# Kernel optimization log

Hardware: AMD Instinct MI355X
Metric: run time of the kernel (lower is better)

The kernel has to match this reference:

```python
import jax, jax.numpy as jnp
import numpy as np

N_USERS = 50000
N_ENT = 100000
N_NODES = N_USERS + N_ENT
N_EDGES = 2400000
EMB = 64
LAYER_DIMS = [(64, 64), (64, 32), (32, 16)]  # (in_dim, out_dim) per layer


def setup_inputs() -> dict:
    key = jax.random.key(0)
    ks = jax.random.split(key, 20)
    inp = {
        'user_embed': jax.random.normal(ks[0], (N_USERS, EMB), jnp.float32) * 0.1,
        'entity_embed': jax.random.normal(ks[1], (N_ENT, EMB), jnp.float32) * 0.1,
        'edge_val': jax.random.uniform(ks[2], (N_EDGES,), jnp.float32),
        'edge_row': jax.random.randint(ks[3], (N_EDGES,), 0, N_NODES),
        'edge_col': jax.random.randint(ks[4], (N_EDGES,), 0, N_NODES),
    }
    i = 5
    for k, (din, dout) in enumerate(LAYER_DIMS):
        scale = float(np.sqrt(6.0 / (din + dout)))  # xavier_uniform
        inp[f'W_gc_{k}'] = jax.random.uniform(ks[i], (din, dout), jnp.float32, -scale, scale); i += 1
        inp[f'b_gc_{k}'] = jnp.zeros((dout,), jnp.float32)
        inp[f'W_bi_{k}'] = jax.random.uniform(ks[i], (din, dout), jnp.float32, -scale, scale); i += 1
        inp[f'b_bi_{k}'] = jnp.zeros((dout,), jnp.float32)
    return inp


def _l2_normalize(x):
    # matches F.normalize(x, p=2, dim=1) with eps=1e-12
    return x / jnp.maximum(jnp.linalg.norm(x, axis=1, keepdims=True), 1e-12)


def reference(user_embed, entity_embed, edge_val, edge_row, edge_col,
              W_gc_0, b_gc_0, W_bi_0, b_bi_0,
              W_gc_1, b_gc_1, W_bi_1, b_bi_1,
              W_gc_2, b_gc_2, W_bi_2, b_bi_2):
    layers = [(W_gc_0, b_gc_0, W_bi_0, b_bi_0),
              (W_gc_1, b_gc_1, W_bi_1, b_bi_1),
              (W_gc_2, b_gc_2, W_bi_2, b_bi_2)]
    x = jnp.concatenate([user_embed, entity_embed], axis=0)  # [N, 64]
    all_emb = [x]
    for W_gc, b_gc, W_bi, b_bi in layers:
        # sparse A @ x : gather source features, scale by edge value, segment-sum into rows
        msgs = edge_val[:, None] * x[edge_col]                       # [E, d]
        side = jax.ops.segment_sum(msgs, edge_row, num_segments=N_NODES)  # [N, d]
        sum_emb = jax.nn.leaky_relu((x + side) @ W_gc + b_gc)        # GCN path
        bi_emb = jax.nn.leaky_relu((x * side) @ W_bi + b_bi)         # bi-interaction path
        x = _l2_normalize(sum_emb + bi_emb)                          # dropout p=0 (eval)
        all_emb.append(x)
    all_emb = jnp.concatenate(all_emb, axis=1)  # [N, 64+64+32+16]
    return all_emb[:N_USERS], all_emb[N_USERS:]
```

## Files before the change

### kernel.cpp

```cpp
#include <hip/hip_runtime.h>
#include <hip/hip_fp16.h>

constexpr int N_USERS = 50000;
constexpr int N_ENT   = 100000;
constexpr int N_NODES = 150000;
constexpr int N_EDGES = 2400000;
constexpr int OUT_D   = 176;

constexpr int NBKT      = 293;
constexpr int P1_BLOCKS = 293;
constexpr int CHUNK     = 8192;
constexpr int TBL       = NBKT * P1_BLOCKS;
constexpr int SCAN_BLKS = (TBL + 1023) / 1024;


typedef _Float16 h2v __attribute__((ext_vector_type(2)));
union H2U { unsigned u; h2v v; };

__device__ inline float dot2(unsigned a, unsigned b, float c) {
    H2U x, y; x.u = a; y.u = b;
    return __builtin_amdgcn_fdot2(x.v, y.v, c, false);
}

__global__ __launch_bounds__(256) void init_x_kernel(const float* __restrict__ ue,
                                                     const float* __restrict__ ee,
                                                     float* __restrict__ out,
                                                     __half* __restrict__ xh) {
    int tid = blockIdx.x * 256 + threadIdx.x;
    int n = tid >> 4, q = tid & 15;
    const float* src = (n < N_USERS) ? ue + (size_t)n * 64
                                     : ee + (size_t)(n - N_USERS) * 64;
    float4 v = *(const float4*)(src + q * 4);
    *(float4*)(out + (size_t)n * OUT_D + q * 4) = v;
    union { __half2 h[2]; uint2 u; } pk;
    pk.h[0] = __floats2half2_rn(v.x, v.y);
    pk.h[1] = __floats2half2_rn(v.z, v.w);
    *(uint2*)(xh + (size_t)n * 64 + q * 4) = pk.u;
}

__global__ __launch_bounds__(256) void conv_kernel(const float* __restrict__ src,
                                                   __half* __restrict__ xh, int DIN) {
    int tid = blockIdx.x * 256 + threadIdx.x;
    int n = tid / (DIN / 2), t = tid % (DIN / 2);
    float2 v = *(const float2*)(src + (size_t)n * OUT_D + 2 * t);
    *(__half2*)(xh + (size_t)n * DIN + 2 * t) = __floats2half2_rn(v.x, v.y);
}

__global__ __launch_bounds__(256) void wt_kernel(const float* __restrict__ Wg0,
                                                 const float* __restrict__ Wb0,
                                                 const float* __restrict__ Wg1,
                                                 const float* __restrict__ Wb1,
                                                 const float* __restrict__ Wg2,
                                                 const float* __restrict__ Wb2,
                                                 __half* __restrict__ WT) {
    int idx = blockIdx.x * 256 + threadIdx.x;
    const float* src; int dout, base;
    if (idx < 8192)       { base = (idx < 4096) ? 0 : 4096;
                            src  = (idx < 4096) ? Wg0 : Wb0;  dout = 64; }
    else if (idx < 12288) { base = (idx < 10240) ? 8192 : 10240;
                            src  = (idx < 10240) ? Wg1 : Wb1; dout = 32; }
    else                  { base = (idx < 12800) ? 12288 : 12800;
                            src  = (idx < 12800) ? Wg2 : Wb2; dout = 16; }
    int r = idx - base;
    int i = r / dout, o = r % dout;
    int dest = base + (i / 8) * dout * 8 + o * 8 + (i % 8);
    WT[dest] = __float2half(src[r]);
}

__global__ __launch_bounds__(256) void histP1_kernel(const int* __restrict__ er,
                                                     int* __restrict__ table) {
    __shared__ int h[NBKT];
    for (int i = threadIdx.x; i < NBKT; i += 256) h[i] = 0;
    __syncthreads();
    int base = blockIdx.x * CHUNK;
    for (int i = threadIdx.x; i < CHUNK; i += 256) {
        int e = base + i;
        if (e < N_EDGES) atomicAdd(&h[er[e] >> 9], 1);
    }
    __syncthreads();
    for (int i = threadIdx.x; i < NBKT; i += 256)
        table[i * P1_BLOCKS + blockIdx.x] = h[i];
}

__global__ __launch_bounds__(1024) void scanA_kernel(const int* __restrict__ a,
                                                     int* __restrict__ bsum, int n) {
    __shared__ int wsum[16];
    int i = blockIdx.x * 1024 + threadIdx.x;
    int v = (i < n) ? a[i] : 0;
    #pragma unroll
    for (int off = 32; off; off >>= 1) v += __shfl_xor(v, off);
    int lane = threadIdx.x & 63, w = threadIdx.x >> 6;
    if (lane == 0) wsum[w] = v;
    __syncthreads();
    if (threadIdx.x == 0) {
        int t = 0;
        #pragma unroll
        for (int k = 0; k < 16; ++k) t += wsum[k];
        bsum[blockIdx.x] = t;
    }
}

__global__ __launch_bounds__(1024) void scanB_kernel(int* __restrict__ bsum, int n) {
    __shared__ int wtot[16];
    __shared__ int carry_s;
    int tid = threadIdx.x;
    int lane = tid & 63, w = tid >> 6;
    if (tid == 0) carry_s = 0;
    __syncthreads();
    for (int base = 0; base < n; base += 1024) {
        int i = base + tid;
        int v = (i < n) ? bsum[i] : 0;
        int incl = v;
        #pragma unroll
        for (int off = 1; off < 64; off <<= 1) {
            int t = __shfl_up(incl, off);
            if (lane >= off) incl += t;
        }
        if (lane == 63) wtot[w] = incl;
        __syncthreads();
        int woff = 0, total = 0;
        #pragma unroll
        for (int k = 0; k < 16; ++k) {
            int tk = wtot[k];
            if (k < w) woff += tk;
            total += tk;
        }
        if (i < n) bsum[i] = carry_s + woff + incl - v;
        __syncthreads();
        if (tid == 0) carry_s += total;
        __syncthreads();
    }
}

__global__ __launch_bounds__(1024) void scanC_kernel(int* __restrict__ a,
                                                     const int* __restrict__ bsum, int n) {
    __shared__ int wtot[16];
    int i = blockIdx.x * 1024 + threadIdx.x;
    int lane = threadIdx.x & 63, w = threadIdx.x >> 6;
    int v = (i < n) ? a[i] : 0;
    int incl = v;
    #pragma unroll
    for (int off = 1; off < 64; off <<= 1) {
        int t = __shfl_up(incl, off);
        if (lane >= off) incl += t;
    }
    if (lane == 63) wtot[w] = incl;
    __syncthreads();
    int woff = 0;
    #pragma unroll
    for (int k = 0; k < 16; ++k) if (k < w) woff += wtot[k];
    if (i < n) a[i] = bsum[blockIdx.x] + woff + incl - v;
}

__global__ __launch_bounds__(256) void scatterP1_kernel(const float* __restrict__ ev,
                                                        const int*   __restrict__ er,
                                                        const int*   __restrict__ ec,
                                                        const int*   __restrict__ table,
                                                        unsigned long long* __restrict__ tmp) {
    __shared__ int lcur[NBKT];
    for (int i = threadIdx.x; i < NBKT; i += 256)
        lcur[i] = table[i * P1_BLOCKS + blockIdx.x];
    __syncthreads();
    int base = blockIdx.x * CHUNK;
    for (int i = threadIdx.x; i < CHUNK; i += 256) {
        int e = base + i;
        if (e < N_EDGES) {
            int r = er[e], c = ec[e];
            unsigned hb = (unsigned)__half_as_ushort(__float2half_rn(ev[e]));
            unsigned v14 = (hb + 2u) >> 2;
            int pos = atomicAdd(&lcur[r >> 9], 1);
            tmp[pos] = ((unsigned long long)(r & 511) << 32)
                     | ((unsigned)c << 14) | v14;
        }
    }
}

__global__ __launch_bounds__(512) void pass2_kernel(const unsigned long long* __restrict__ tmp,
                                                    const int* __restrict__ table,
                                                    unsigned* __restrict__ edges,
                                                    int* __restrict__ cursor) {
    __shared__ int hcnt[512];
    __shared__ int sinc[512];
    __shared__ int lcur[512];
    int b = blockIdx.x;
    int tid = threadIdx.x;
    int eStart = table[b * P1_BLOCKS];
    int eEnd = (b + 1 < NBKT) ? table[(b + 1) * P1_BLOCKS] : N_EDGES;

    hcnt[tid] = 0;
    __syncthreads();
    for (int e = eStart + tid; e < eEnd; e += 512)
        atomicAdd(&hcnt[(int)(tmp[e] >> 32)], 1);
    __syncthreads();
    sinc[tid] = hcnt[tid];
    __syncthreads();
    #pragma unroll
    for (int off = 1; off < 512; off <<= 1) {
        int t = (tid >= off) ? sinc[tid - off] : 0;
        __syncthreads();
        sinc[tid] += t;
        __syncthreads();
    }
    int row = b * 512 + tid;
    if (row < N_NODES) cursor[row] = eStart + sinc[tid];
    lcur[tid] = eStart + sinc[tid] - hcnt[tid];
    __syncthreads();
    for (int e = eStart + tid; e < eEnd; e += 512) {
        unsigned long long rec = tmp[e];
        int pos = atomicAdd(&lcur[(int)(rec >> 32)], 1);
        edges[pos] = (unsigned)rec;
    }
}

template<int DIN, int DOUT>
__global__ __launch_bounds__(256, 4) void fused_layer_kernel(
        const int*          __restrict__ cursor,
        const unsigned int* __restrict__ edges,
        const __half*       __restrict__ xh,
        float* __restrict__ out,
        const __half* __restrict__ WT, int wgOff, int wbOff,
        const float* __restrict__ bgc, const float* __restrict__ bbi,
        int cin, int cout) {
    __shared__ unsigned ash[4][DIN / 2];
    __shared__ unsigned bsh[4][DIN / 2];

    int tid = threadIdx.x;
    int w = tid >> 6, lane = tid & 63;
    int n = blockIdx.x * 4 + w;

    constexpr int QP = DIN / 4;
    constexpr int NE = 64 / QP;
    int g = lane / QP;
    int t = lane % QP;

    int s = n ? cursor[n - 1] : 0;
    int e_end = cursor[n];

    float4 xv = make_float4(0.f, 0.f, 0.f, 0.f);
    if (lane < QP) xv = *(const float4*)(out + (size_t)n * OUT_D + cin + 4 * lane);

    const uint2* xq = (const uint2*)xh;
    float fx0 = 0.f, fx1 = 0.f, fx2 = 0.f, fx3 = 0.f;

    for (int e = s; e < e_end; e += 8 * NE) {
        unsigned ue[8];
        #pragma unroll
        for (int j = 0; j < 8; ++j) {
            int i = e + j * NE + g;
            unsigned raw = edges[i];
            ue[j] = (i < e_end) ? raw : 0u;
        }
        uint2 xx[8];
        #pragma unroll
        for (int j = 0; j < 8; ++j)
            xx[j] = xq[(size_t)(ue[j] >> 14) * QP + t];

        __half2 a0 = __floats2half2_rn(0.f, 0.f);
        __half2 a1 = a0;
        #pragma unroll
        for (int j = 0; j < 8; ++j) {
            unsigned bits = (ue[j] & 0x3FFFu) << 2;
            __half vh = __ushort_as_half((unsigned short)bits);
            __half2 vv2 = __half2half2(vh);
            a0 = __hfma2(vv2, *(__half2*)&xx[j].x, a0);
            a1 = __hfma2(vv2, *(__half2*)&xx[j].y, a1);
            if (j == 3 || j == 7) {
                float2 f0 = __half22float2(a0);
                float2 f1 = __half22float2(a1);
                fx0 += f0.x; fx1 += f0.y; fx2 += f1.x; fx3 += f1.y;
                a0 = __floats2half2_rn(0.f, 0.f); a1 = a0;
            }
        }
    }
    #pragma unroll
    for (int m = 32; m >= QP; m >>= 1) {
        fx0 += __shfl_xor(fx0, m);
        fx1 += __shfl_xor(fx1, m);
        fx2 += __shfl_xor(fx2, m);
        fx3 += __shfl_xor(fx3, m);
    }

    if (lane < QP) {
        __half2 a01 = __floats2half2_rn(xv.x + fx0, xv.y + fx1);
        __half2 a23 = __floats2half2_rn(xv.z + fx2, xv.w + fx3);
        __half2 b01 = __floats2half2_rn(xv.x * fx0, xv.y * fx1);
        __half2 b23 = __floats2half2_rn(xv.z * fx2, xv.w * fx3);
        ash[w][2 * lane]     = *(unsigned*)&a01;
        ash[w][2 * lane + 1] = *(unsigned*)&a23;
        bsh[w][2 * lane]     = *(unsigned*)&b01;
        bsh[w][2 * lane + 1] = *(unsigned*)&b23;
    }
    __syncthreads();

    float hres = 0.f;
    if constexpr (DOUT == DIN) {
        int o = lane;
        uint4 wg[DIN / 8], wb[DIN / 8];
        #pragma unroll
        for (int k = 0; k < DIN / 8; ++k) {
            wg[k] = *(const uint4*)(WT + wgOff + (size_t)(k * DOUT + o) * 8);
            wb[k] = *(const uint4*)(WT + wbOff + (size_t)(k * DOUT + o) * 8);
        }
        float ag = bgc[o], ab = bbi[o];
        #pragma unroll
        for (int k = 0; k < DIN / 8; ++k) {
            uint4 a4 = *(const uint4*)&ash[w][k * 4];
            uint4 b4 = *(const uint4*)&bsh[w][k * 4];
            ag = dot2(a4.x, wg[k].x, ag); ag = dot2(a4.y, wg[k].y, ag);
            ag = dot2(a4.z, wg[k].z, ag); ag = dot2(a4.w, wg[k].w, ag);
            ab = dot2(b4.x, wb[k].x, ab); ab = dot2(b4.y, wb[k].y, ab);
            ab = dot2(b4.z, wb[k].z, ab); ab = dot2(b4.w, wb[k].w, ab);
        }
        ag = ag > 0.f ? ag : 0.01f * ag;
        ab = ab > 0.f ? ab : 0.01f * ab;
        hres = ag + ab;
    } else {
        int o = lane & (DOUT - 1);
        bool gc = lane < DOUT;
        bool active = lane < 2 * DOUT;
        int woff2 = gc ? wgOff : wbOff;
        uint4 wr[DIN / 8];
        #pragma unroll
        for (int k = 0; k < DIN / 8; ++k)
            wr[k] = *(const uint4*)(WT + woff2 + (size_t)(k * DOUT + o) * 8);
        const unsigned* sp = gc ? &ash[w][0] : &bsh[w][0];
        float own = active ? (gc ? bgc[o] : bbi[o]) : 0.f;
        #pragma unroll
        for (int k = 0; k < DIN / 8; ++k) {
            uint4 s4 = *(const uint4*)(sp + k * 4);
            own = dot2(s4.x, wr[k].x, own); own = dot2(s4.y, wr[k].y, own);
            own = dot2(s4.z, wr[k].z, own); own = dot2(s4.w, wr[k].w, own);
        }
        own = own > 0.f ? own : 0.01f * own;
        float other = __shfl_xor(own, DOUT);
        hres = own + other;
    }

    float hq = (lane < DOUT) ? hres : 0.f;
    float ss = hq * hq;
    #pragma unroll
    for (int off = 32; off; off >>= 1) ss += __shfl_xor(ss, off);

    if (lane < DOUT) {
        float inv = 1.f / fmaxf(sqrtf(ss), 1e-12f);
        out[(size_t)n * OUT_D + cout + lane] = hres * inv;
    }
}

extern "C" void kernel_launch(void* const* d_in, const int* in_sizes, int n_in,
                              void* d_out, int out_size, void* d_ws, size_t ws_size,
                              hipStream_t stream) {
    const float* ue = (const float*)d_in[0];
    const float* ee = (const float*)d_in[1];
    const float* ev = (const float*)d_in[2];
    const int*   er = (const int*)d_in[3];
    const int*   ec = (const int*)d_in[4];
    float* out = (float*)d_out;

    unsigned long long* tmp    = (unsigned long long*)d_ws;
    __half*             xh     = (__half*)d_ws;
    unsigned int*       edges  = (unsigned int*)((char*)d_ws + 19200000);
    int*                cursor = (int*)((char*)d_ws + 28800000);
    int*                table  = (int*)((char*)d_ws + 29400000);
    int*                bsum   = (int*)((char*)d_ws + 30000000);
    __half*             WT     = (__half*)((char*)d_ws + 30100000);

    histP1_kernel<<<P1_BLOCKS, 256, 0, stream>>>(er, table);
    scanA_kernel<<<SCAN_BLKS, 1024, 0, stream>>>(table, bsum, TBL);
    scanB_kernel<<<1, 1024, 0, stream>>>(bsum, SCAN_BLKS);
    scanC_kernel<<<SCAN_BLKS, 1024, 0, stream>>>(table, bsum, TBL);
    scatterP1_kernel<<<P1_BLOCKS, 256, 0, stream>>>(ev, er, ec, table, tmp);
    pass2_kernel<<<NBKT, 512, 0, stream>>>(tmp, table, edges, cursor);

    init_x_kernel<<<(N_NODES * 16) / 256, 256, 0, stream>>>(ue, ee, out, xh);
    wt_kernel<<<52, 256, 0, stream>>>((const float*)d_in[5],  (const float*)d_in[7],
                                      (const float*)d_in[9],  (const float*)d_in[11],
                                      (const float*)d_in[13], (const float*)d_in[15], WT);

    const int GRID = N_NODES / 4;

    fused_layer_kernel<64, 64><<<GRID, 256, 0, stream>>>(cursor, edges, xh, out,
        WT, 0, 4096, (const float*)d_in[6], (const float*)d_in[8], 0, 64);
    conv_kernel<<<(N_NODES * 32) / 256, 256, 0, stream>>>(out + 64, xh, 64);

    fused_layer_kernel<64, 32><<<GRID, 256, 0, stream>>>(cursor, edges, xh, out,
        WT, 8192, 10240, (const float*)d_in[10], (const float*)d_in[12], 64, 128);
    conv_kernel<<<(N_NODES * 16) / 256, 256, 0, stream>>>(out + 128, xh, 32);

    fused_layer_kernel<32, 16><<<GRID, 256, 0, stream>>>(cursor, edges, xh, out,
        WT, 12288, 12800, (const float*)d_in[14], (const float*)d_in[16], 128, 160);
}
```

Measured before the change: 401.3 us.

## Use fixed-point edge weights, fp32 accumulation, and a 16-edge unrolled gather

Edge values are now stored as 14-bit fixed point instead of truncated fp16 bits. The gather loop accumulates in fp32 rather than packed half FMAs. The main loop handles 16 edges per step with wave-uniform bounds taken via readfirstlane, and only the tail iteration keeps bounds masking. Launch bounds go up to 8 waves per SIMD to raise occupancy. This trades packed-half math for more fp32 FMAs and conversions, and the higher occupancy target may cause register spills.

```diff
diff --git a/kernel.cpp b/kernel.cpp
--- a/kernel.cpp
+++ b/kernel.cpp
@@ -166,11 +166,11 @@
         int e = base + i;
         if (e < N_EDGES) {
             int r = er[e], c = ec[e];
-            unsigned hb = (unsigned)__half_as_ushort(__float2half_rn(ev[e]));
-            unsigned v14 = (hb + 2u) >> 2;
+            int v14 = (int)(ev[e] * 16384.0f + 0.5f);
+            v14 = v14 > 16383 ? 16383 : v14;
             int pos = atomicAdd(&lcur[r >> 9], 1);
             tmp[pos] = ((unsigned long long)(r & 511) << 32)
-                     | ((unsigned)c << 14) | v14;
+                     | ((unsigned)c << 14) | (unsigned)v14;
         }
     }
 }
@@ -213,7 +213,7 @@
 }
 
 template<int DIN, int DOUT>
-__global__ __launch_bounds__(256, 4) void fused_layer_kernel(
+__global__ __launch_bounds__(256, 8) void fused_layer_kernel(
         const int*          __restrict__ cursor,
         const unsigned int* __restrict__ edges,
         const __half*       __restrict__ xh,
@@ -230,65 +230,77 @@
 
     constexpr int QP = DIN / 4;
     constexpr int NE = 64 / QP;
+    constexpr int DEPTH = 16 / NE;
     int g = lane / QP;
     int t = lane % QP;
 
-    int s = n ? cursor[n - 1] : 0;
+    int s0 = n ? cursor[n - 1] : 0;
     int e_end = cursor[n];
+    int sS = __builtin_amdgcn_readfirstlane(s0);
+    int sE = __builtin_amdgcn_readfirstlane(e_end);
 
     float4 xv = make_float4(0.f, 0.f, 0.f, 0.f);
     if (lane < QP) xv = *(const float4*)(out + (size_t)n * OUT_D + cin + 4 * lane);
 
     const uint2* xq = (const uint2*)xh;
-    float fx0 = 0.f, fx1 = 0.f, fx2 = 0.f, fx3 = 0.f;
-
-    for (int e = s; e < e_end; e += 8 * NE) {
-        unsigned ue[8];
-        #pragma unroll
-        for (int j = 0; j < 8; ++j) {
+    float a0 = 0.f, a1 = 0.f, a2 = 0.f, a3 = 0.f;
+
+    int e = sS;
+    for (; e + 16 <= sE; e += 16) {
+        unsigned ue[DEPTH];
+        #pragma unroll
+        for (int j = 0; j < DEPTH; ++j) ue[j] = edges[e + j * NE + g];
+        uint2 xx[DEPTH];
+        #pragma unroll
+        for (int j = 0; j < DEPTH; ++j)
+            xx[j] = xq[(size_t)(ue[j] >> 14) * QP + t];
+        #pragma unroll
+        for (int j = 0; j < DEPTH; ++j) {
+            float f = (float)(ue[j] & 16383u) * (1.0f / 16384.0f);
+            float2 flo = __half22float2(*(__half2*)&xx[j].x);
+            float2 fhi = __half22float2(*(__half2*)&xx[j].y);
+            a0 += f * flo.x; a1 += f * flo.y;
+            a2 += f * fhi.x; a3 += f * fhi.y;
+        }
+    }
+    if (e < sE) {
+        unsigned ue[DEPTH];
+        #pragma unroll
+        for (int j = 0; j < DEPTH; ++j) {
             int i = e + j * NE + g;
             unsigned raw = edges[i];
             ue[j] = (i < e_end) ? raw : 0u;
         }
-        uint2 xx[8];
-        #pragma unroll
-        for (int j = 0; j < 8; ++j)
+        uint2 xx[DEPTH];
+        #pragma unroll
+        for (int j = 0; j < DEPTH; ++j)
             xx[j] = xq[(size_t)(ue[j] >> 14) * QP + t];
-
-        __half2 a0 = __floats2half2_rn(0.f, 0.f);
-        __half2 a1 = a0;
-        #pragma unroll
-        for (int j = 0; j < 8; ++j) {
-            unsigned bits = (ue[j] & 0x3FFFu) << 2;
-            __half vh = __ushort_as_half((unsigned short)bits);
-            __half2 vv2 = __half2half2(vh);
-            a0 = __hfma2(vv2, *(__half2*)&xx[j].x, a0);
-            a1 = __hfma2(vv2, *(__half2*)&xx[j].y, a1);
-            if (j == 3 || j == 7) {
-                float2 f0 = __half22float2(a0);
-                float2 f1 = __half22float2(a1);
-                fx0 += f0.x; fx1 += f0.y; fx2 += f1.x; fx3 += f1.y;
-                a0 = __floats2half2_rn(0.f, 0.f); a1 = a0;
-            }
+        #pragma unroll
+        for (int j = 0; j < DEPTH; ++j) {
+            float f = (float)(ue[j] & 16383u) * (1.0f / 16384.0f);
+            float2 flo = __half22float2(*(__half2*)&xx[j].x);
+            float2 fhi = __half22float2(*(__half2*)&xx[j].y);
+            a0 += f * flo.x; a1 += f * flo.y;
+            a2 += f * fhi.x; a3 += f * fhi.y;
         }
     }
     #pragma unroll
     for (int m = 32; m >= QP; m >>= 1) {
-        fx0 += __shfl_xor(fx0, m);
-        fx1 += __shfl_xor(fx1, m);
-        fx2 += __shfl_xor(fx2, m);
-        fx3 += __shfl_xor(fx3, m);
+        a0 += __shfl_xor(a0, m);
+        a1 += __shfl_xor(a1, m);
+        a2 += __shfl_xor(a2, m);
+        a3 += __shfl_xor(a3, m);
     }
 
     if (lane < QP) {
-        __half2 a01 = __floats2half2_rn(xv.x + fx0, xv.y + fx1);
-        __half2 a23 = __floats2half2_rn(xv.z + fx2, xv.w + fx3);
-        __half2 b01 = __floats2half2_rn(xv.x * fx0, xv.y * fx1);
-        __half2 b23 = __floats2half2_rn(xv.z * fx2, xv.w * fx3);
-        ash[w][2 * lane]     = *(unsigned*)&a01;
-        ash[w][2 * lane + 1] = *(unsigned*)&a23;
-        bsh[w][2 * lane]     = *(unsigned*)&b01;
-        bsh[w][2 * lane + 1] = *(unsigned*)&b23;
+        __half2 A01 = __floats2half2_rn(xv.x + a0, xv.y + a1);
+        __half2 A23 = __floats2half2_rn(xv.z + a2, xv.w + a3);
+        __half2 B01 = __floats2half2_rn(xv.x * a0, xv.y * a1);
+        __half2 B23 = __floats2half2_rn(xv.z * a2, xv.w * a3);
+        ash[w][2 * lane]     = *(unsigned*)&A01;
+        ash[w][2 * lane + 1] = *(unsigned*)&A23;
+        bsh[w][2 * lane]     = *(unsigned*)&B01;
+        bsh[w][2 * lane + 1] = *(unsigned*)&B23;
     }
     __syncthreads();
 
```

Result: faster. 383.9 us (-4.3%).
